# Kernel optimization log

Measured on AMD Instinct MI355X. Metric: run time of the kernel, lower is better.

## Reference

```python
import jax, jax.numpy as jnp
import numpy as np

# ---- straight-through binary quantizers (custom VJP matches torch autograd.Functions) ----
@jax.custom_vjp
def bq(x):
    return jnp.sign(x)
def _bq_fwd(x):
    return jnp.sign(x), x
def _bq_bwd(x, g):
    return (g * ((x > -1.0) & (x < 1.0)).astype(g.dtype),)
bq.defvjp(_bq_fwd, _bq_bwd)

@jax.custom_vjp
def bq_quad(x):
    return jnp.sign(x)
def _bqq_fwd(x):
    return jnp.sign(x), x
def _bqq_bwd(x, g):
    return (jnp.maximum(2.0 - jnp.abs(2.0 * x), 0.0) * g,)
bq_quad.defvjp(_bqq_fwd, _bqq_bwd)

def bilinear(x, W, s, b):
    # BiLinear: row-centered sign weights scaled by learned per-row factor, sign activations
    Wc = W - jnp.mean(W, axis=-1, keepdims=True)
    Wb = s * bq(Wc)                      # (out, in)
    return bq(x) @ Wb.T + b

def selective_scan(u, delta, A, Bs, Cs, D, delta_bias):
    # u, delta: (B,K,Dn,L); A: (K,Dn,N); Bs,Cs: (B,K,N,L); D, delta_bias: (K,Dn)
    Bn, K, Dn, L = u.shape
    N = A.shape[-1]
    delta = jax.nn.softplus(delta + delta_bias[None, :, :, None])
    def step(h, inp):
        ut, dt, Bt, Ct = inp             # (B,K,Dn),(B,K,Dn),(B,K,N),(B,K,N)
        dA = jnp.exp(dt[..., None] * A[None])
        h = dA * h + (dt * ut)[..., None] * Bt[:, :, None, :]
        y = jnp.einsum('bkdn,bkn->bkd', h, Ct)
        return h, y
    h0 = jnp.zeros((Bn, K, Dn, N), u.dtype)
    _, ys = jax.lax.scan(step, h0,
                         (u.transpose(3, 0, 1, 2), delta.transpose(3, 0, 1, 2),
                          Bs.transpose(3, 0, 1, 2), Cs.transpose(3, 0, 1, 2)))
    y = ys.transpose(1, 2, 3, 0)         # (B,K,Dn,L)
    return y + D[None, :, :, None] * u

def _forward(x, W_in, b_in, s_in, move0_b, conv_W, conv_b, rp_b0, prelu_a, rp_b1,
             Wl, bl, sl, Wd, bd, sd, dt_bias, A_logs, Ds, ln_w, ln_b, W_out, b_out, s_out):
    Bn, H, Wi, dm = x.shape
    Dn = conv_W.shape[0]
    K = 4
    N = A_logs.shape[1]
    R = Wd.shape[2]
    L = H * Wi
    xz = bilinear(x, W_in, s_in, b_in)                  # (B,H,W,2*Dn)
    xp, z = jnp.split(xz, 2, axis=-1)
    xc = xp.transpose(0, 3, 1, 2)                       # (B,Dn,H,W)
    # BConv2d: move0 bias -> sign (quad STE) -> binary conv -> RPReLU -> residual
    t = bq_quad(xc + move0_b[None, :, None, None])
    sc = jax.lax.stop_gradient(jnp.mean(jnp.abs(conv_W), axis=(1, 2, 3), keepdims=True))
    cw = jnp.clip(conv_W, -1.0, 1.0)
    Wb = jax.lax.stop_gradient(sc * jnp.sign(conv_W) - cw) + cw
    t = jax.lax.conv_general_dilated(t, Wb, (1, 1), [(1, 1), (1, 1)],
                                     dimension_numbers=('NCHW', 'OIHW', 'NCHW'))
    t = t + conv_b[None, :, None, None]
    t = t + rp_b0[None, :, None, None]
    t = jnp.where(t >= 0, t, prelu_a[None, :, None, None] * t)
    t = t + rp_b1[None, :, None, None] + xc
    xconv = jax.nn.silu(t)
    # 4-direction scan inputs
    x_flat = xconv.reshape(Bn, Dn, L)
    x_tr = xconv.transpose(0, 1, 3, 2).reshape(Bn, Dn, L)
    x_hwwh = jnp.stack([x_flat, x_tr], axis=1)
    xs = jnp.concatenate([x_hwwh, jnp.flip(x_hwwh, axis=-1)], axis=1)   # (B,K,Dn,L)
    # NOTE: torch does .view(B,L,-1) on contiguous (B,Dn,L) slices = raw reshape (not transpose)
    xin = xs.reshape(Bn, K, L, Dn)
    x_dbl = jax.vmap(bilinear, in_axes=(1, 0, 0, 0), out_axes=1)(xin, Wl, sl, bl)  # (B,K,L,R+2N)
    x_dbl = x_dbl.transpose(0, 1, 3, 2)                                 # (B,K,R+2N,L)
    dts_r, Bs, Cs = jnp.split(x_dbl, [R, R + N], axis=2)
    dts_in = dts_r.reshape(Bn, K, L, R)  # raw reshape, matches torch .view
    dts = jax.vmap(bilinear, in_axes=(1, 0, 0, 0), out_axes=1)(dts_in, Wd, sd, bd)  # (B,K,L,Dn)
    dts = dts.transpose(0, 1, 3, 2)                                     # (B,K,Dn,L)
    A = -jnp.exp(A_logs).reshape(K, Dn, N)
    out_y = selective_scan(xs, dts, A, Bs, Cs, Ds.reshape(K, Dn), dt_bias.reshape(K, Dn))
    inv_y = jnp.flip(out_y[:, 2:4], axis=-1)
    wh_y = out_y[:, 1].reshape(Bn, Dn, Wi, H).transpose(0, 1, 3, 2).reshape(Bn, Dn, L)
    invwh_y = inv_y[:, 1].reshape(Bn, Dn, Wi, H).transpose(0, 1, 3, 2).reshape(Bn, Dn, L)
    y = out_y[:, 0] + inv_y[:, 0] + wh_y + invwh_y                      # (B,Dn,L)
    y = y.transpose(0, 2, 1).reshape(Bn, H, Wi, Dn)
    mu = jnp.mean(y, axis=-1, keepdims=True)
    var = jnp.var(y, axis=-1, keepdims=True)
    y = (y - mu) / jnp.sqrt(var + 1e-5) * ln_w + ln_b                   # LayerNorm eps=1e-5
    y = y * jax.nn.silu(z)
    return bilinear(y, W_out, s_out, b_out)

def setup_inputs():
    key = jax.random.key(0)
    ks = jax.random.split(key, 12)
    B, H, Wi, dm = 4, 64, 64, 96
    Dn, N, R, K = 192, 16, 6, 4
    u = lambda k, sh, a: jax.random.uniform(k, sh, jnp.float32, -a, a)
    x = jax.random.normal(ks[0], (B, H, Wi, dm), jnp.float32)
    W_in = u(ks[1], (2 * Dn, dm), 0.015)
    b_in = u(ks[2], (2 * Dn,), 0.01)
    s_in = jnp.mean(jnp.abs(W_in), axis=1, keepdims=True)
    move0_b = jnp.zeros((Dn,), jnp.float32)
    conv_W = 0.05 * jax.random.normal(ks[3], (Dn, Dn, 3, 3), jnp.float32)
    conv_b = u(ks[4], (Dn,), 0.01)
    rp_b0 = jnp.zeros((Dn,), jnp.float32)
    prelu_a = 0.25 * jnp.ones((Dn,), jnp.float32)
    rp_b1 = jnp.zeros((Dn,), jnp.float32)
    Wl = u(ks[5], (K, R + 2 * N, Dn), 0.015)
    bl = u(ks[6], (K, R + 2 * N), 0.01)
    sl = jnp.mean(jnp.abs(Wl), axis=2, keepdims=True)
    std = R ** -0.5
    Wd = u(ks[7], (K, Dn, R), std)
    bd = u(ks[8], (K, Dn), 0.01)
    sd = jnp.mean(jnp.abs(Wd), axis=2, keepdims=True)
    dt = jnp.exp(jax.random.uniform(ks[9], (K * Dn,), jnp.float32)
                 * (np.log(0.1) - np.log(0.001)) + np.log(0.001))
    dt = jnp.clip(dt, 1e-4, None)
    dt_bias = dt + jnp.log(-jnp.expm1(-dt))
    A_logs = jnp.tile(jnp.log(jnp.arange(1, N + 1, dtype=jnp.float32))[None, :], (K * Dn, 1))
    Ds = jnp.ones((K * Dn,), jnp.float32)
    ln_w = jnp.ones((Dn,), jnp.float32)
    ln_b = jnp.zeros((Dn,), jnp.float32)
    W_out = u(ks[10], (dm, Dn), 0.015)
    b_out = u(ks[11], (dm,), 0.01)
    s_out = jnp.mean(jnp.abs(W_out), axis=1, keepdims=True)
    return dict(x=x, W_in=W_in, b_in=b_in, s_in=s_in, move0_b=move0_b, conv_W=conv_W,
                conv_b=conv_b, rp_b0=rp_b0, prelu_a=prelu_a, rp_b1=rp_b1, Wl=Wl, bl=bl,
                sl=sl, Wd=Wd, bd=bd, sd=sd, dt_bias=dt_bias, A_logs=A_logs, Ds=Ds,
                ln_w=ln_w, ln_b=ln_b, W_out=W_out, b_out=b_out, s_out=s_out)

def reference(x, W_in, b_in, s_in, move0_b, conv_W, conv_b, rp_b0, prelu_a, rp_b1,
              Wl, bl, sl, Wd, bd, sd, dt_bias, A_logs, Ds, ln_w, ln_b, W_out, b_out, s_out):
    return _forward(x, W_in, b_in, s_in, move0_b, conv_W, conv_b, rp_b0, prelu_a, rp_b1,
                    Wl, bl, sl, Wd, bd, sd, dt_bias, A_logs, Ds, ln_w, ln_b, W_out, b_out, s_out)
```

## Files before the change

kernel.cpp:

```cpp
#include <hip/hip_runtime.h>
#include <math.h>
#include <stdint.h>

#define BB 4
#define HH 64
#define WW2 64
#define DM 96
#define DN 192
#define KK 4
#define NN 16
#define RR 6
#define LL 4096
#define RN 38

#define LOG2E 1.4426950408889634f
#define LN2   0.6931471805599453f

#define OFF_WDB      0
#define OFF_WCS      4608
#define OFF_WAUX     15360
#define OFF_WSC      16896
#define OFF_WBIB     17088
#define OFF_WOUTB    18240
#define OFF_WLBB     18816
#define OFF_XBP      19728
#define OFF_PXS      19728
#define OFF_PXIN     412944
#define OFF_XP       462096
#define OFF_XCONV    3607824
#define OFF_XCT      6753552
#define OFF_HEND     462096
#define OFF_YA       9899280
#define OFF_SSUM     22482192

#define PLANE 4356
#define NCH 128
#define CHUNK 32

__device__ __forceinline__ float softplusf(float v) {
  return fmaxf(v, 0.f) + LN2 * log2f(1.f + exp2f(-fabsf(v) * LOG2E));
}
__device__ __forceinline__ float siluf(float v) {
  return v / (1.f + expf(-v));
}
__device__ __forceinline__ float waveAllSum(float s) {
  #pragma unroll
  for (int off = 32; off; off >>= 1) s += __shfl_xor(s, off, 64);
  return s;
}

__global__ __launch_bounds__(64) void k_prep(
    const float* __restrict__ W_in, const float* __restrict__ s_in,
    const float* __restrict__ W_out, const float* __restrict__ s_out,
    const float* __restrict__ Wl, const float* __restrict__ sl,
    const float* __restrict__ Wd, const float* __restrict__ sd,
    const float* __restrict__ convW, float* __restrict__ ws) {
  __shared__ float srow[1728];
  int r = blockIdx.x, lane = threadIdx.x;
  if (r < 384) {
    const float* row = W_in + r * DM;
    float s = 0.f;
    for (int c = lane; c < DM; c += 64) s += row[c];
    s = waveAllSum(s);
    float mean = s / (float)DM;
    if (lane < 3) {
      uint32_t wv = 0;
      #pragma unroll
      for (int i = 0; i < 32; ++i) wv |= (row[lane * 32 + i] - mean > 0.f ? 1u : 0u) << i;
      ((uint32_t*)(ws + OFF_WBIB))[r * 3 + lane] = wv;
    }
  } else if (r < 480) {
    int m = r - 384;
    const float* row = W_out + m * DN;
    float s = 0.f;
    for (int c = lane; c < DN; c += 64) s += row[c];
    s = waveAllSum(s);
    float mean = s / (float)DN;
    if (lane < 6) {
      uint32_t wv = 0;
      #pragma unroll
      for (int i = 0; i < 32; ++i) wv |= (row[lane * 32 + i] - mean > 0.f ? 1u : 0u) << i;
      ((uint32_t*)(ws + OFF_WOUTB))[m * 6 + lane] = wv;
    }
  } else if (r < 632) {
    int idx = r - 480;
    const float* row = Wl + idx * DN;
    float s = 0.f;
    for (int c = lane; c < DN; c += 64) s += row[c];
    s = waveAllSum(s);
    float mean = s / (float)DN;
    if (lane < 6) {
      uint32_t wv = 0;
      #pragma unroll
      for (int i = 0; i < 32; ++i) wv |= (row[lane * 32 + i] - mean > 0.f ? 1u : 0u) << i;
      ((uint32_t*)(ws + OFF_WLBB))[idx * 6 + lane] = wv;
    }
  } else if (r < 1400) {
    int idx = r - 632;
    const float* row = Wd + idx * RR;
    float s = (lane < RR) ? row[lane] : 0.f;
    s = waveAllSum(s);
    float mean = s / (float)RR;
    unsigned long long mb = __ballot((lane < RR) && (row[lane] - mean > 0.f));
    if (lane == 0) {
      ((uint32_t*)(ws + OFF_WDB))[idx] = (uint32_t)mb & 0x3Fu;
      (ws + OFF_WDB)[768 + idx] = sd[idx];
    }
  } else if (r < 1592) {
    int o = r - 1400;
    const float* row = convW + o * 1728;
    float s = 0.f;
    for (int j = lane; j < 1728; j += 64) {
      float v = row[j];
      srow[j] = v;
      s += fabsf(v);
    }
    s = waveAllSum(s);
    __syncthreads();
    float sc = s / 1728.f;
    uint32_t* wb = (uint32_t*)(ws + OFF_WCS);
    int* aux = (int*)(ws + OFF_WAUX);
    float* scf = ws + OFF_WSC;
    uint32_t word = 0;
    if (lane < 54) {
      int cw = lane / 9, tap = lane % 9;
      #pragma unroll
      for (int i = 0; i < 32; ++i)
        word |= (srow[(cw * 32 + i) * 9 + tap] > 0.f ? 1u : 0u) << i;
      wb[o * 56 + lane] = word;
    } else if (lane < 56) {
      wb[o * 56 + lane] = 0u;
    }
    int pc = (lane < 54) ? 2 * (int)__popc(word) - 32 : 0;
    int tapid = lane % 9;
    int wst = 0;
    #pragma unroll
    for (int cw = 0; cw < 6; ++cw) wst += __shfl(pc, cw * 9 + tapid, 64);
    int w_t[9];
    #pragma unroll
    for (int t9 = 0; t9 < 9; ++t9) w_t[t9] = __shfl(wst, t9, 64);
    if (lane == 0) {
      aux[o * 8 + 0] = w_t[0] + w_t[3] + w_t[6];
      aux[o * 8 + 1] = w_t[2] + w_t[5] + w_t[8];
      aux[o * 8 + 2] = w_t[0] + w_t[1] + w_t[2];
      aux[o * 8 + 3] = w_t[6] + w_t[7] + w_t[8];
      aux[o * 8 + 4] = w_t[0];
      aux[o * 8 + 5] = w_t[2];
      aux[o * 8 + 6] = w_t[6];
      aux[o * 8 + 7] = w_t[8];
      scf[o] = sc;
    }
  } else {
    int p = r - 1592;
    uint32_t* plane = (uint32_t*)(ws + OFF_XBP) + (size_t)p * PLANE;
    for (int i = lane; i < 66; i += 64) {
      plane[i] = 0u;
      plane[65 * 66 + i] = 0u;
    }
    for (int i = lane; i < 64; i += 64) {
      plane[(i + 1) * 66] = 0u;
      plane[(i + 1) * 66 + 65] = 0u;
    }
  }
}

__global__ __launch_bounds__(384) void k_bilin_in(
    const float* __restrict__ x, const float* __restrict__ b_in,
    const float* __restrict__ s_in, const float* __restrict__ move0,
    const float* __restrict__ ws, float* __restrict__ xp,
    uint32_t* __restrict__ pxin, uint32_t* __restrict__ xb) {
  __shared__ uint32_t spx[16 * 3];
  __shared__ float sxz[192 * 17];
  __shared__ float smv[DN];
  int p0 = blockIdx.x * 16;
  if (threadIdx.x < 48) {
    int pix = threadIdx.x / 3, wd = threadIdx.x % 3;
    const float* base = x + (size_t)(p0 + pix) * DM + wd * 32;
    uint32_t wv = 0;
    #pragma unroll
    for (int i = 0; i < 32; ++i) wv |= (base[i] > 0.f ? 1u : 0u) << i;
    spx[pix * 3 + wd] = wv;
  }
  if (threadIdx.x < DN) smv[threadIdx.x] = move0[threadIdx.x];
  __syncthreads();
  int half = threadIdx.x / 192;
  int o = threadIdx.x - half * 192;
  uint32_t w0, w1, w2;
  {
    const uint32_t* wb = (const uint32_t*)(ws + OFF_WBIB) + o * 3;
    w0 = wb[0]; w1 = wb[1]; w2 = wb[2];
  }
  float bias = b_in[o], sc = s_in[o];
  #pragma unroll
  for (int pp = 0; pp < 8; ++pp) {
    int pix = half * 8 + pp;
    int P = (int)__popc(spx[pix * 3 + 0] ^ w0) + (int)__popc(spx[pix * 3 + 1] ^ w1) +
            (int)__popc(spx[pix * 3 + 2] ^ w2);
    sxz[o * 17 + pix] = bias + sc * (float)(DM - 2 * P);
  }
  __syncthreads();
  int b = p0 >> 12, l0 = p0 & 4095;
  for (int f = threadIdx.x; f < DN * 16; f += 384) {
    int od = f >> 4, pix = f & 15;
    xp[((size_t)(b * DN + od)) * LL + l0 + pix] = sxz[od * 17 + pix];
  }
  if (threadIdx.x < 48) {
    int pix = threadIdx.x / 3, wd = threadIdx.x % 3;
    pxin[(size_t)(p0 + pix) * 3 + wd] = spx[pix * 3 + wd];
  }
  if (threadIdx.x < 96) {
    int pix = threadIdx.x / 6, cw = threadIdx.x % 6;
    uint32_t wv = 0;
    #pragma unroll
    for (int i = 0; i < 32; ++i) {
      int dch = cw * 32 + i;
      wv |= ((sxz[dch * 17 + pix] + smv[dch] > 0.f) ? 1u : 0u) << i;
    }
    int l = l0 + pix, h = l >> 6, w = l & 63;
    uint32_t* plane = xb + (size_t)(b * 6 + cw) * PLANE;
    plane[(h + 1) * 66 + 1 + w] = wv;
  }
}

__global__ __launch_bounds__(256) void k_conv(
    const uint32_t* __restrict__ xb, const float* __restrict__ xc,
    const uint32_t* __restrict__ wbits, const int* __restrict__ aux,
    const float* __restrict__ scf, const float* __restrict__ conv_b,
    const float* __restrict__ rp_b0, const float* __restrict__ prelu_a,
    const float* __restrict__ rp_b1, float* __restrict__ xconv) {
  int og = blockIdx.x & 3;
  int stripe = (blockIdx.x >> 2) & 15;
  int b = blockIdx.x >> 6;
  int w = threadIdx.x & 63, r = threadIdx.x >> 6;
  int h = stripe * 4 + r;

  __shared__ uint32_t swb[48 * 56];
  __shared__ int saux[48 * 8];
  __shared__ float sconst[48 * 4];
  for (int i = threadIdx.x; i < 48 * 56; i += 256) swb[i] = wbits[og * (48 * 56) + i];
  for (int i = threadIdx.x; i < 48 * 8; i += 256) saux[i] = aux[og * (48 * 8) + i];
  if (threadIdx.x < 48) {
    int o = og * 48 + threadIdx.x;
    sconst[threadIdx.x * 4 + 0] = scf[o];
    sconst[threadIdx.x * 4 + 1] = conv_b[o] + rp_b0[o];
    sconst[threadIdx.x * 4 + 2] = prelu_a[o];
    sconst[threadIdx.x * 4 + 3] = rp_b1[o];
  }

  uint32_t xw[6][9];
  const uint32_t* xpb = xb + (size_t)b * 6 * PLANE;
  #pragma unroll
  for (int cw = 0; cw < 6; ++cw) {
    const uint32_t* plane = xpb + cw * PLANE + (h + 1) * 66 + (w + 1);
    #pragma unroll
    for (int dy = 0; dy < 3; ++dy) {
      #pragma unroll
      for (int dx = 0; dx < 3; ++dx)
        xw[cw][dy * 3 + dx] = plane[(dy - 1) * 66 + (dx - 1)];
    }
  }
  bool isL = (w == 0), isR = (w == 63);
  bool isT = (h == 0), isB = (h == 63);
  const float* xcp = xc + ((size_t)(b * DN + og * 48)) * LL + h * 64 + w;
  float* xop = xconv + ((size_t)(b * DN + og * 48)) * LL + h * 64 + w;
  __syncthreads();

  #pragma unroll 1
  for (int oc = 0; oc < 48; ++oc) {
    const uint32_t* wp = &swb[oc * 56];
    int P = 0;
    #pragma unroll
    for (int cw = 0; cw < 6; ++cw) {
      int pp = 0;
      #pragma unroll
      for (int t = 0; t < 9; ++t) pp += (int)__popc(wp[cw * 9 + t] ^ xw[cw][t]);
      P += pp;
    }
    int corr = isL ? saux[oc * 8 + 0] : (isR ? saux[oc * 8 + 1] : 0);
    if (isT) {
      corr += saux[oc * 8 + 2];
      if (isL) corr -= saux[oc * 8 + 4];
      if (isR) corr -= saux[oc * 8 + 5];
    }
    if (isB) {
      corr += saux[oc * 8 + 3];
      if (isL) corr -= saux[oc * 8 + 6];
      if (isR) corr -= saux[oc * 8 + 7];
    }
    float acc = sconst[oc * 4 + 0] * (float)(1728 - 2 * P + corr);
    float t = acc + sconst[oc * 4 + 1];
    t = (t >= 0.f) ? t : sconst[oc * 4 + 2] * t;
    t += sconst[oc * 4 + 3] + *xcp;
    *xop = siluf(t);
    xcp += LL; xop += LL;
  }
}

__global__ __launch_bounds__(256) void k_build_bits(const float* __restrict__ xconv,
                                                    uint32_t* __restrict__ pxs) {
  __shared__ float tile[64][65];
  int bd = blockIdx.x;
  int b = bd / DN, dch = bd - b * DN;
  const float* img = xconv + (size_t)bd * LL;
  for (int i = threadIdx.x; i < LL; i += 256)
    tile[i >> 6][i & 63] = img[i];
  __syncthreads();
  int lane = threadIdx.x & 63;
  #pragma unroll
  for (int k = 0; k < 4; ++k) {
    size_t wbase = ((size_t)((b * KK + k) * DN + dch)) * 128;
    for (int j = threadIdx.x; j < LL; j += 256) {
      float v;
      if (k == 0)      v = tile[j >> 6][j & 63];
      else if (k == 1) v = tile[j & 63][j >> 6];
      else if (k == 2) { int t2 = 4095 - j; v = tile[t2 >> 6][t2 & 63]; }
      else             { int t2 = 4095 - j; v = tile[t2 & 63][t2 >> 6]; }
      unsigned long long m = __ballot(v > 0.f);
      if (lane == 0)       pxs[wbase + (j >> 5)] = (uint32_t)m;
      else if (lane == 32) pxs[wbase + (j >> 5)] = (uint32_t)(m >> 32);
    }
  }
}

__global__ __launch_bounds__(256) void k_xpose(const float* __restrict__ xconv,
                                               float* __restrict__ xct) {
  __shared__ float tile[64][65];
  int ts = blockIdx.x & 63;
  int rest = blockIdx.x >> 6;
  int dg = rest % 3;
  int b = rest / 3;
  int d0 = dg * 64, t0 = ts * 64;
  for (int i = threadIdx.x; i < 4096; i += 256) {
    int dd = i >> 6, tt = i & 63;
    tile[dd][tt] = xconv[((size_t)(b * DN + d0 + dd)) * LL + t0 + tt];
  }
  __syncthreads();
  for (int i = threadIdx.x; i < 4096; i += 256) {
    int tt = i >> 6, dd = i & 63;
    xct[((size_t)(b * LL + t0 + tt)) * DN + d0 + dd] = tile[dd][tt];
  }
}

__device__ __forceinline__ void rpowers(float r, float* a) {
  float r2 = r * r, r3 = r2 * r, r4 = r2 * r2, r8 = r4 * r4;
  a[0] = r;       a[1] = r2;      a[2] = r3;      a[3] = r4;
  a[4] = r4 * r;  a[5] = r4 * r2; a[6] = r4 * r3; a[7] = r8;
  a[8] = r8 * r;  a[9] = r8 * r2; a[10] = r8 * r3; a[11] = r8 * r4;
  a[12] = r8 * a[4]; a[13] = r8 * a[5]; a[14] = r8 * a[6]; a[15] = r8 * r8;
}

__global__ __launch_bounds__(192) void k_scan_a(
    const float* __restrict__ xct, const uint32_t* __restrict__ pxs,
    const float* __restrict__ ws, const float* __restrict__ bl,
    const float* __restrict__ sl, const float* __restrict__ bd,
    const float* __restrict__ dt_bias, const float* __restrict__ A_logs,
    const float* __restrict__ Ds, float* __restrict__ yA,
    float* __restrict__ hend, float* __restrict__ Ssum) {
  int c = blockIdx.x & (NCH - 1);
  int bk = blockIdx.x >> 7;
  int k = bk & 3, b = bk >> 2;
  int d = threadIdx.x;
  int t0 = c << 5;
  __shared__ uint32_t sdtm[CHUNK];
  __shared__ uint32_t spxr[CHUNK * 6];
  __shared__ uint32_t swl[RN * 6];
  __shared__ float sblv[RN], sslv[RN];
  __shared__ float4 sB4[CHUNK * 4];
  __shared__ float4 sC4[CHUNK * 4];
  __shared__ float sDV[7 * 192], sR[7 * 192];
  float* sBf = (float*)sB4;
  float* sCf = (float*)sC4;
  const uint32_t* ppx = pxs + (size_t)bk * 24576;
  spxr[d] = ppx[t0 * 6 + d];
  for (int i = d; i < RN * 6; i += 192) swl[i] = ((const uint32_t*)(ws + OFF_WLBB))[k * RN * 6 + i];
  if (d < RN) {
    sblv[d] = bl[k * RN + d];
    sslv[d] = sl[k * RN + d];
  }
  __syncthreads();
  if (d < CHUNK) {
    uint32_t m = 0;
    int fbase = (t0 + d) * 6;
    #pragma unroll
    for (int r = 0; r < 6; ++r) {
      int f = fbase + r;
      int o = f >> 12, l = f & 4095;
      const uint32_t* prow = ppx + l * 6;
      int P = 0;
      #pragma unroll
      for (int j = 0; j < 6; ++j) P += (int)__popc(prow[j] ^ swl[o * 6 + j]);
      float val = sblv[o] + sslv[o] * (float)(DN - 2 * P);
      m |= (val > 0.f ? 1u : 0u) << r;
    }
    sdtm[d] = m;
  }
  for (int i = d; i < CHUNK * 32; i += 192) {
    int t = i >> 5, nn = i & 31;
    int o = RR + nn;
    int P = 0;
    #pragma unroll
    for (int j = 0; j < 6; ++j) P += (int)__popc(spxr[t * 6 + j] ^ swl[o * 6 + j]);
    float val = sblv[o] + sslv[o] * (float)(DN - 2 * P);
    if (nn < 16) sBf[t * 16 + nn] = val;
    else         sCf[t * 16 + (nn - 16)] = val;
  }
  uint32_t w6 = ((const uint32_t*)(ws + OFF_WDB))[k * DN + d];
  float sdv = (ws + OFF_WDB)[768 + k * DN + d];
  float biasd = bd[k * DN + d] + dt_bias[k * DN + d];
  float Dd = Ds[k * DN + d];
  #pragma unroll
  for (int pc = 0; pc < 7; ++pc) {
    float dv = softplusf(biasd + sdv * (float)(RR - 2 * pc));
    sDV[pc * 192 + d] = dv;
    sR[pc * 192 + d] = exp2f(-dv * LOG2E);
  }
  float Araw[16];
  bool fok = true;
  {
    const float* ap = A_logs + (k * DN + d) * NN;
    #pragma unroll
    for (int n = 0; n < NN; ++n) {
      Araw[n] = -expf(ap[n]);
      fok = fok && (fabsf(Araw[n] + (float)(n + 1)) < 1e-3f);
    }
  }
  bool fastpath = (__ballot(fok) == ~0ull);
  float An[16];
  if (!fastpath) {
    #pragma unroll
    for (int n = 0; n < NN; ++n) An[n] = Araw[n] * LOG2E;
  }
  float h[16];
  #pragma unroll
  for (int n = 0; n < NN; ++n) h[n] = 0.f;
  float S = 0.f;
  int ubase = b * (LL * DN) + d;
  int ybase = bk * (LL * DN) + d;
  __syncthreads();
  #pragma unroll 1
  for (int seg = 0; seg < 4; ++seg) {
    float uu[8];
    int r192[8];
    #pragma unroll
    for (int i = 0; i < 8; ++i) {
      int t = t0 + seg * 8 + i;
      int r = (k >= 2) ? (4095 - t) : t;
      if (k & 1) r = ((r & 63) << 6) | (r >> 6);
      r192[i] = r * DN;
      uu[i] = xct[ubase + r192[i]];
    }
    #pragma unroll
    for (int i = 0; i < 8; ++i) {
      int t = seg * 8 + i;
      float uv = uu[i];
      int pc = (int)__popc(sdtm[t] ^ w6);
      float dv = sDV[pc * 192 + d];
      S += dv;
      float du = dv * uv;
      float yv = Dd * uv;
      if (fastpath) {
        float rv = sR[pc * 192 + d];
        float a[16];
        rpowers(rv, a);
        #pragma unroll
        for (int g = 0; g < 4; ++g) {
          float4 bv = sB4[t * 4 + g];
          float4 cv = sC4[t * 4 + g];
          h[4 * g + 0] = a[4 * g + 0] * h[4 * g + 0] + du * bv.x;
          h[4 * g + 1] = a[4 * g + 1] * h[4 * g + 1] + du * bv.y;
          h[4 * g + 2] = a[4 * g + 2] * h[4 * g + 2] + du * bv.z;
          h[4 * g + 3] = a[4 * g + 3] * h[4 * g + 3] + du * bv.w;
          yv += cv.x * h[4 * g + 0];
          yv += cv.y * h[4 * g + 1];
          yv += cv.z * h[4 * g + 2];
          yv += cv.w * h[4 * g + 3];
        }
      } else {
        #pragma unroll
        for (int g = 0; g < 4; ++g) {
          float4 bv = sB4[t * 4 + g];
          float4 cv = sC4[t * 4 + g];
          float a0 = exp2f(dv * An[4 * g + 0]);
          float a1 = exp2f(dv * An[4 * g + 1]);
          float a2 = exp2f(dv * An[4 * g + 2]);
          float a3 = exp2f(dv * An[4 * g + 3]);
          h[4 * g + 0] = a0 * h[4 * g + 0] + du * bv.x;
          h[4 * g + 1] = a1 * h[4 * g + 1] + du * bv.y;
          h[4 * g + 2] = a2 * h[4 * g + 2] + du * bv.z;
          h[4 * g + 3] = a3 * h[4 * g + 3] + du * bv.w;
          yv += cv.x * h[4 * g + 0];
          yv += cv.y * h[4 * g + 1];
          yv += cv.z * h[4 * g + 2];
          yv += cv.w * h[4 * g + 3];
        }
      }
      yA[ybase + r192[i]] = yv;
    }
  }
  float* hp = hend + (size_t)c * 49152 + (size_t)(bk * DN + d) * 16;
  #pragma unroll
  for (int n = 0; n < NN; n += 4)
    *(float4*)(hp + n) = make_float4(h[n], h[n + 1], h[n + 2], h[n + 3]);
  Ssum[c * 3072 + bk * DN + d] = S;
}

__global__ __launch_bounds__(256) void k_scan_b(
    const float* __restrict__ A_logs, const float* __restrict__ Ssum,
    float* __restrict__ hend) {
  int tid = blockIdx.x * 256 + threadIdx.x;
  int bkd = tid >> 4, n = tid & 15;
  int bk = bkd / DN, d = bkd - bk * DN;
  int k = bk & 3;
  float An2 = -expf(A_logs[(k * DN + d) * NN + n]) * LOG2E;
  float h = 0.f;
  float Sc = Ssum[bkd];
  float he = hend[tid];
  #pragma unroll 1
  for (int c = 0; c < NCH; ++c) {
    float Sn = 0.f, hn = 0.f;
    if (c < NCH - 1) {
      Sn = Ssum[(c + 1) * 3072 + bkd];
      hn = hend[(size_t)(c + 1) * 49152 + tid];
    }
    hend[(size_t)c * 49152 + tid] = h;
    h = exp2f(An2 * Sc) * h + he;
    Sc = Sn; he = hn;
  }
}

__global__ __launch_bounds__(192) void k_scan_corr(
    float* __restrict__ yA, const uint32_t* __restrict__ pxs,
    const float* __restrict__ ws, const float* __restrict__ bl,
    const float* __restrict__ sl, const float* __restrict__ bd,
    const float* __restrict__ dt_bias, const float* __restrict__ A_logs,
    const float* __restrict__ h0buf) {
  int c = blockIdx.x & (NCH - 1);
  if (c == 0) return;
  int bk = blockIdx.x >> 7;
  int k = bk & 3;
  int d = threadIdx.x;
  int t0 = c << 5;
  __shared__ uint32_t sdtm[CHUNK];
  __shared__ uint32_t spxr[CHUNK * 6];
  __shared__ uint32_t swl[RN * 6];
  __shared__ float sblv[RN], sslv[RN];
  __shared__ float4 sC4[CHUNK * 4];
  __shared__ float sDV[7 * 192];
  float* sCf = (float*)sC4;
  const uint32_t* ppx = pxs + (size_t)bk * 24576;
  spxr[d] = ppx[t0 * 6 + d];
  for (int i = d; i < RN * 6; i += 192) swl[i] = ((const uint32_t*)(ws + OFF_WLBB))[k * RN * 6 + i];
  if (d < RN) {
    sblv[d] = bl[k * RN + d];
    sslv[d] = sl[k * RN + d];
  }
  __syncthreads();
  if (d < CHUNK) {
    uint32_t m = 0;
    int fbase = (t0 + d) * 6;
    #pragma unroll
    for (int r = 0; r < 6; ++r) {
      int f = fbase + r;
      int o = f >> 12, l = f & 4095;
      const uint32_t* prow = ppx + l * 6;
      int P = 0;
      #pragma unroll
      for (int j = 0; j < 6; ++j) P += (int)__popc(prow[j] ^ swl[o * 6 + j]);
      float val = sblv[o] + sslv[o] * (float)(DN - 2 * P);
      m |= (val > 0.f ? 1u : 0u) << r;
    }
    sdtm[d] = m;
  }
  for (int i = d; i < CHUNK * 16; i += 192) {
    int t = i >> 4, n = i & 15;
    int o = RR + NN + n;
    int P = 0;
    #pragma unroll
    for (int j = 0; j < 6; ++j) P += (int)__popc(spxr[t * 6 + j] ^ swl[o * 6 + j]);
    sCf[t * 16 + n] = sblv[o] + sslv[o] * (float)(DN - 2 * P);
  }
  uint32_t w6 = ((const uint32_t*)(ws + OFF_WDB))[k * DN + d];
  float sdv = (ws + OFF_WDB)[768 + k * DN + d];
  float biasd = bd[k * DN + d] + dt_bias[k * DN + d];
  #pragma unroll
  for (int pc = 0; pc < 7; ++pc)
    sDV[pc * 192 + d] = softplusf(biasd + sdv * (float)(RR - 2 * pc));
  float Araw[16];
  bool fok = true;
  {
    const float* ap = A_logs + (k * DN + d) * NN;
    #pragma unroll
    for (int n = 0; n < NN; ++n) {
      Araw[n] = -expf(ap[n]);
      fok = fok && (fabsf(Araw[n] + (float)(n + 1)) < 1e-3f);
    }
  }
  bool fastpath = (__ballot(fok) == ~0ull);
  float An[16];
  if (!fastpath) {
    #pragma unroll
    for (int n = 0; n < NN; ++n) An[n] = Araw[n] * LOG2E;
  }
  float h0[16];
  {
    const float* hp = h0buf + (size_t)c * 49152 + (size_t)(bk * DN + d) * 16;
    #pragma unroll
    for (int n = 0; n < NN; n += 4) {
      float4 v = *(const float4*)(hp + n);
      h0[n] = v.x; h0[n + 1] = v.y; h0[n + 2] = v.z; h0[n + 3] = v.w;
    }
  }
  float S = 0.f;
  int ybase = bk * (LL * DN) + d;
  __syncthreads();
  #pragma unroll 1
  for (int seg = 0; seg < 4; ++seg) {
    float yy[8];
    int r192[8];
    #pragma unroll
    for (int i = 0; i < 8; ++i) {
      int t = t0 + seg * 8 + i;
      int r = (k >= 2) ? (4095 - t) : t;
      if (k & 1) r = ((r & 63) << 6) | (r >> 6);
      r192[i] = r * DN;
      yy[i] = yA[ybase + r192[i]];
    }
    #pragma unroll
    for (int i = 0; i < 8; ++i) {
      int t = seg * 8 + i;
      int pc = (int)__popc(sdtm[t] ^ w6);
      S += sDV[pc * 192 + d];
      float yv = 0.f;
      if (fastpath) {
        float rho = exp2f(-S * LOG2E);
        float a[16];
        rpowers(rho, a);
        #pragma unroll
        for (int g = 0; g < 4; ++g) {
          float4 cv = sC4[t * 4 + g];
          yv += cv.x * (a[4 * g + 0] * h0[4 * g + 0]);
          yv += cv.y * (a[4 * g + 1] * h0[4 * g + 1]);
          yv += cv.z * (a[4 * g + 2] * h0[4 * g + 2]);
          yv += cv.w * (a[4 * g + 3] * h0[4 * g + 3]);
        }
      } else {
        #pragma unroll
        for (int g = 0; g < 4; ++g) {
          float4 cv = sC4[t * 4 + g];
          yv += cv.x * (exp2f(S * An[4 * g + 0]) * h0[4 * g + 0]);
          yv += cv.y * (exp2f(S * An[4 * g + 1]) * h0[4 * g + 1]);
          yv += cv.z * (exp2f(S * An[4 * g + 2]) * h0[4 * g + 2]);
          yv += cv.w * (exp2f(S * An[4 * g + 3]) * h0[4 * g + 3]);
        }
      }
      yA[ybase + r192[i]] = yy[i] + yv;
    }
  }
}

__global__ __launch_bounds__(256) void k_ln_out(
    const float* __restrict__ yA, const uint32_t* __restrict__ pxin,
    const float* __restrict__ b_in, const float* __restrict__ s_in,
    const float* __restrict__ ln_w, const float* __restrict__ ln_b,
    const float* __restrict__ ws, const float* __restrict__ b_out,
    const float* __restrict__ s_out, float* __restrict__ out) {
  __shared__ float ty[64 * 193];
  __shared__ float ps[256];
  __shared__ float smu[64], srs[64];
  __shared__ float slw[DN], slb[DN];
  __shared__ uint32_t ybits[64 * 6];
  __shared__ uint32_t swo[96 * 6];
  __shared__ float sb[96], ssc[96];
  __shared__ uint32_t szw[DN * 3];
  __shared__ float szb[DN], szs[DN];
  __shared__ uint32_t spxt[64 * 3];
  int b = blockIdx.x >> 6;
  int l0 = (blockIdx.x & 63) << 6;
  if (threadIdx.x < DN) {
    slw[threadIdx.x] = ln_w[threadIdx.x];
    slb[threadIdx.x] = ln_b[threadIdx.x];
    szb[threadIdx.x] = b_in[DN + threadIdx.x];
    szs[threadIdx.x] = s_in[DN + threadIdx.x];
  }
  for (int i = threadIdx.x; i < 96 * 6; i += 256) swo[i] = ((const uint32_t*)(ws + OFF_WOUTB))[i];
  for (int i = threadIdx.x; i < DN * 3; i += 256) szw[i] = ((const uint32_t*)(ws + OFF_WBIB))[DN * 3 + i];
  if (threadIdx.x < 96) {
    sb[threadIdx.x] = b_out[threadIdx.x];
    ssc[threadIdx.x] = s_out[threadIdx.x];
  }
  for (int i = threadIdx.x; i < 192; i += 256) spxt[i] = pxin[(size_t)(b * LL + l0) * 3 + i];
  const float* y0 = yA + (size_t)(b * 4 + 0) * (LL * DN) + (size_t)l0 * DN;
  const float* y1 = yA + (size_t)(b * 4 + 1) * (LL * DN) + (size_t)l0 * DN;
  const float* y2 = yA + (size_t)(b * 4 + 2) * (LL * DN) + (size_t)l0 * DN;
  const float* y3 = yA + (size_t)(b * 4 + 3) * (LL * DN) + (size_t)l0 * DN;
  for (int i = threadIdx.x; i < 64 * DN; i += 256) {
    int lc = i / DN, dd = i - lc * DN;
    size_t off = (size_t)lc * DN + dd;
    ty[lc * 193 + dd] = y0[off] + y1[off] + y2[off] + y3[off];
  }
  __syncthreads();
  int lc = threadIdx.x & 63, part = threadIdx.x >> 6;
  float s = 0.f;
  for (int d = part * 48; d < part * 48 + 48; ++d) s += ty[lc * 193 + d];
  ps[threadIdx.x] = s;
  __syncthreads();
  if (threadIdx.x < 64)
    smu[threadIdx.x] = (ps[threadIdx.x] + ps[threadIdx.x + 64] +
                        ps[threadIdx.x + 128] + ps[threadIdx.x + 192]) / (float)DN;
  __syncthreads();
  float mu = smu[lc];
  float q = 0.f;
  for (int d = part * 48; d < part * 48 + 48; ++d) {
    float v = ty[lc * 193 + d] - mu; q += v * v;
  }
  ps[threadIdx.x] = q;
  __syncthreads();
  if (threadIdx.x < 64) {
    float var = (ps[threadIdx.x] + ps[threadIdx.x + 64] +
                 ps[threadIdx.x + 128] + ps[threadIdx.x + 192]) / (float)DN;
    srs[threadIdx.x] = rsqrtf(var + 1e-5f);
  }
  __syncthreads();
  for (int item = threadIdx.x; item < 64 * 6; item += 256) {
    int lc2 = item / 6, wd = item - (item / 6) * 6;
    float mu2 = smu[lc2], rs2 = srs[lc2];
    uint32_t px0 = spxt[lc2 * 3 + 0], px1 = spxt[lc2 * 3 + 1], px2 = spxt[lc2 * 3 + 2];
    uint32_t wv = 0;
    #pragma unroll
    for (int i = 0; i < 32; ++i) {
      int dd = wd * 32 + i;
      float lnv = (ty[lc2 * 193 + dd] - mu2) * rs2 * slw[dd] + slb[dd];
      int P = (int)__popc(px0 ^ szw[dd * 3 + 0]) + (int)__popc(px1 ^ szw[dd * 3 + 1]) +
              (int)__popc(px2 ^ szw[dd * 3 + 2]);
      float zv = szb[dd] + szs[dd] * (float)(DM - 2 * P);
      wv |= ((lnv * zv > 0.f) ? 1u : 0u) << i;
    }
    ybits[lc2 * 6 + wd] = wv;
  }
  __syncthreads();
  float* op = out + (size_t)(b * LL + l0) * DM;
  for (int oi = threadIdx.x; oi < 64 * DM; oi += 256) {
    int pr = oi / DM, m = oi % DM;
    int P = 0;
    #pragma unroll
    for (int j = 0; j < 6; ++j) P += (int)__popc(ybits[pr * 6 + j] ^ swo[m * 6 + j]);
    op[(size_t)pr * DM + m] = sb[m] + ssc[m] * (float)(DN - 2 * P);
  }
}

extern "C" void kernel_launch(void* const* d_in, const int* in_sizes, int n_in,
                              void* d_out, int out_size, void* d_ws, size_t ws_size,
                              hipStream_t stream) {
  const float* x       = (const float*)d_in[0];
  const float* W_in    = (const float*)d_in[1];
  const float* b_in    = (const float*)d_in[2];
  const float* s_in    = (const float*)d_in[3];
  const float* move0_b = (const float*)d_in[4];
  const float* conv_W  = (const float*)d_in[5];
  const float* conv_b  = (const float*)d_in[6];
  const float* rp_b0   = (const float*)d_in[7];
  const float* prelu_a = (const float*)d_in[8];
  const float* rp_b1   = (const float*)d_in[9];
  const float* Wl      = (const float*)d_in[10];
  const float* bl      = (const float*)d_in[11];
  const float* sl      = (const float*)d_in[12];
  const float* Wd      = (const float*)d_in[13];
  const float* bd      = (const float*)d_in[14];
  const float* sd      = (const float*)d_in[15];
  const float* dt_bias = (const float*)d_in[16];
  const float* A_logs  = (const float*)d_in[17];
  const float* Ds      = (const float*)d_in[18];
  const float* ln_w    = (const float*)d_in[19];
  const float* ln_b    = (const float*)d_in[20];
  const float* W_out   = (const float*)d_in[21];
  const float* b_out   = (const float*)d_in[22];
  const float* s_out   = (const float*)d_in[23];
  float* ws  = (float*)d_ws;
  float* out = (float*)d_out;

  hipLaunchKernelGGL(k_prep, dim3(1616), dim3(64), 0, stream,
                     W_in, s_in, W_out, s_out, Wl, sl, Wd, sd, conv_W, ws);
  hipLaunchKernelGGL(k_bilin_in, dim3(1024), dim3(384), 0, stream,
                     x, b_in, s_in, move0_b, ws, ws + OFF_XP,
                     (uint32_t*)(ws + OFF_PXIN), (uint32_t*)(ws + OFF_XBP));
  hipLaunchKernelGGL(k_conv, dim3(256), dim3(256), 0, stream,
                     (const uint32_t*)(ws + OFF_XBP), ws + OFF_XP,
                     (const uint32_t*)(ws + OFF_WCS), (const int*)(ws + OFF_WAUX),
                     ws + OFF_WSC, conv_b, rp_b0, prelu_a, rp_b1,
                     ws + OFF_XCONV);
  hipLaunchKernelGGL(k_build_bits, dim3(768), dim3(256), 0, stream,
                     ws + OFF_XCONV, (uint32_t*)(ws + OFF_PXS));
  hipLaunchKernelGGL(k_xpose, dim3(768), dim3(256), 0, stream,
                     ws + OFF_XCONV, ws + OFF_XCT);
  hipLaunchKernelGGL(k_scan_a, dim3(2048), dim3(192), 0, stream,
                     ws + OFF_XCT, (const uint32_t*)(ws + OFF_PXS), ws, bl, sl,
                     bd, dt_bias, A_logs, Ds, ws + OFF_YA, ws + OFF_HEND,
                     ws + OFF_SSUM);
  hipLaunchKernelGGL(k_scan_b, dim3(192), dim3(256), 0, stream,
                     A_logs, ws + OFF_SSUM, ws + OFF_HEND);
  hipLaunchKernelGGL(k_scan_corr, dim3(2048), dim3(192), 0, stream,
                     ws + OFF_YA, (const uint32_t*)(ws + OFF_PXS), ws, bl, sl,
                     bd, dt_bias, A_logs, ws + OFF_HEND);
  hipLaunchKernelGGL(k_ln_out, dim3(256), dim3(256), 0, stream,
                     ws + OFF_YA, (const uint32_t*)(ws + OFF_PXIN), b_in, s_in,
                     ln_w, ln_b, ws, b_out, s_out, out);
}
```

Before: 324.7 us.

## Split conv and LN-out grids finer and merge bit-build with transpose kernel

The binary conv kernel now splits each 48-channel group into four 12-channel sub-blocks, growing the grid from 256 to 1024 blocks. The LayerNorm/output kernel processes 16 positions per block instead of 64, also giving 1024 blocks, with the reductions reworked to 16-way partial sums. The bit-packing and transpose kernels are merged into one launch that dispatches on block index. The aim is to fill the GPU's compute units better on small grids and to save one launch. The cost is that conv blocks now reload the 54-word input bit window per thread four times as often.

```diff
diff --git a/kernel.cpp b/kernel.cpp
--- a/kernel.cpp
+++ b/kernel.cpp
@@ -228,19 +228,21 @@
     const float* __restrict__ scf, const float* __restrict__ conv_b,
     const float* __restrict__ rp_b0, const float* __restrict__ prelu_a,
     const float* __restrict__ rp_b1, float* __restrict__ xconv) {
-  int og = blockIdx.x & 3;
-  int stripe = (blockIdx.x >> 2) & 15;
-  int b = blockIdx.x >> 6;
+  int ocg = blockIdx.x & 3;
+  int og = (blockIdx.x >> 2) & 3;
+  int stripe = (blockIdx.x >> 4) & 15;
+  int b = blockIdx.x >> 8;
   int w = threadIdx.x & 63, r = threadIdx.x >> 6;
   int h = stripe * 4 + r;
-
-  __shared__ uint32_t swb[48 * 56];
-  __shared__ int saux[48 * 8];
-  __shared__ float sconst[48 * 4];
-  for (int i = threadIdx.x; i < 48 * 56; i += 256) swb[i] = wbits[og * (48 * 56) + i];
-  for (int i = threadIdx.x; i < 48 * 8; i += 256) saux[i] = aux[og * (48 * 8) + i];
-  if (threadIdx.x < 48) {
-    int o = og * 48 + threadIdx.x;
+  int obase = og * 48 + ocg * 12;
+
+  __shared__ uint32_t swb[12 * 56];
+  __shared__ int saux[12 * 8];
+  __shared__ float sconst[12 * 4];
+  for (int i = threadIdx.x; i < 12 * 56; i += 256) swb[i] = wbits[obase * 56 + i];
+  for (int i = threadIdx.x; i < 12 * 8; i += 256) saux[i] = aux[obase * 8 + i];
+  if (threadIdx.x < 12) {
+    int o = obase + threadIdx.x;
     sconst[threadIdx.x * 4 + 0] = scf[o];
     sconst[threadIdx.x * 4 + 1] = conv_b[o] + rp_b0[o];
     sconst[threadIdx.x * 4 + 2] = prelu_a[o];
@@ -261,12 +263,12 @@
   }
   bool isL = (w == 0), isR = (w == 63);
   bool isT = (h == 0), isB = (h == 63);
-  const float* xcp = xc + ((size_t)(b * DN + og * 48)) * LL + h * 64 + w;
-  float* xop = xconv + ((size_t)(b * DN + og * 48)) * LL + h * 64 + w;
+  const float* xcp = xc + ((size_t)(b * DN + obase)) * LL + h * 64 + w;
+  float* xop = xconv + ((size_t)(b * DN + obase)) * LL + h * 64 + w;
   __syncthreads();
 
   #pragma unroll 1
-  for (int oc = 0; oc < 48; ++oc) {
+  for (int oc = 0; oc < 12; ++oc) {
     const uint32_t* wp = &swb[oc * 56];
     int P = 0;
     #pragma unroll
@@ -296,48 +298,48 @@
   }
 }
 
-__global__ __launch_bounds__(256) void k_build_bits(const float* __restrict__ xconv,
-                                                    uint32_t* __restrict__ pxs) {
+__global__ __launch_bounds__(256) void k_bits_xpose(const float* __restrict__ xconv,
+                                                    uint32_t* __restrict__ pxs,
+                                                    float* __restrict__ xct) {
   __shared__ float tile[64][65];
-  int bd = blockIdx.x;
-  int b = bd / DN, dch = bd - b * DN;
-  const float* img = xconv + (size_t)bd * LL;
-  for (int i = threadIdx.x; i < LL; i += 256)
-    tile[i >> 6][i & 63] = img[i];
-  __syncthreads();
-  int lane = threadIdx.x & 63;
-  #pragma unroll
-  for (int k = 0; k < 4; ++k) {
-    size_t wbase = ((size_t)((b * KK + k) * DN + dch)) * 128;
-    for (int j = threadIdx.x; j < LL; j += 256) {
-      float v;
-      if (k == 0)      v = tile[j >> 6][j & 63];
-      else if (k == 1) v = tile[j & 63][j >> 6];
-      else if (k == 2) { int t2 = 4095 - j; v = tile[t2 >> 6][t2 & 63]; }
-      else             { int t2 = 4095 - j; v = tile[t2 & 63][t2 >> 6]; }
-      unsigned long long m = __ballot(v > 0.f);
-      if (lane == 0)       pxs[wbase + (j >> 5)] = (uint32_t)m;
-      else if (lane == 32) pxs[wbase + (j >> 5)] = (uint32_t)(m >> 32);
-    }
-  }
-}
-
-__global__ __launch_bounds__(256) void k_xpose(const float* __restrict__ xconv,
-                                               float* __restrict__ xct) {
-  __shared__ float tile[64][65];
-  int ts = blockIdx.x & 63;
-  int rest = blockIdx.x >> 6;
-  int dg = rest % 3;
-  int b = rest / 3;
-  int d0 = dg * 64, t0 = ts * 64;
-  for (int i = threadIdx.x; i < 4096; i += 256) {
-    int dd = i >> 6, tt = i & 63;
-    tile[dd][tt] = xconv[((size_t)(b * DN + d0 + dd)) * LL + t0 + tt];
-  }
-  __syncthreads();
-  for (int i = threadIdx.x; i < 4096; i += 256) {
-    int tt = i >> 6, dd = i & 63;
-    xct[((size_t)(b * LL + t0 + tt)) * DN + d0 + dd] = tile[dd][tt];
+  if (blockIdx.x < 768) {
+    int bd = blockIdx.x;
+    int b = bd / DN, dch = bd - b * DN;
+    const float* img = xconv + (size_t)bd * LL;
+    for (int i = threadIdx.x; i < LL; i += 256)
+      tile[i >> 6][i & 63] = img[i];
+    __syncthreads();
+    int lane = threadIdx.x & 63;
+    #pragma unroll
+    for (int k = 0; k < 4; ++k) {
+      size_t wbase = ((size_t)((b * KK + k) * DN + dch)) * 128;
+      for (int j = threadIdx.x; j < LL; j += 256) {
+        float v;
+        if (k == 0)      v = tile[j >> 6][j & 63];
+        else if (k == 1) v = tile[j & 63][j >> 6];
+        else if (k == 2) { int t2 = 4095 - j; v = tile[t2 >> 6][t2 & 63]; }
+        else             { int t2 = 4095 - j; v = tile[t2 & 63][t2 >> 6]; }
+        unsigned long long m = __ballot(v > 0.f);
+        if (lane == 0)       pxs[wbase + (j >> 5)] = (uint32_t)m;
+        else if (lane == 32) pxs[wbase + (j >> 5)] = (uint32_t)(m >> 32);
+      }
+    }
+  } else {
+    int idx = blockIdx.x - 768;
+    int ts = idx & 63;
+    int rest = idx >> 6;
+    int dg = rest % 3;
+    int b = rest / 3;
+    int d0 = dg * 64, t0 = ts * 64;
+    for (int i = threadIdx.x; i < 4096; i += 256) {
+      int dd = i >> 6, tt = i & 63;
+      tile[dd][tt] = xconv[((size_t)(b * DN + d0 + dd)) * LL + t0 + tt];
+    }
+    __syncthreads();
+    for (int i = threadIdx.x; i < 4096; i += 256) {
+      int tt = i >> 6, dd = i & 63;
+      xct[((size_t)(b * LL + t0 + tt)) * DN + d0 + dd] = tile[dd][tt];
+    }
   }
 }
 
@@ -664,18 +666,18 @@
     const float* __restrict__ ln_w, const float* __restrict__ ln_b,
     const float* __restrict__ ws, const float* __restrict__ b_out,
     const float* __restrict__ s_out, float* __restrict__ out) {
-  __shared__ float ty[64 * 193];
+  __shared__ float ty[16 * 193];
   __shared__ float ps[256];
-  __shared__ float smu[64], srs[64];
+  __shared__ float smu[16], srs[16];
   __shared__ float slw[DN], slb[DN];
-  __shared__ uint32_t ybits[64 * 6];
+  __shared__ uint32_t ybits[16 * 6];
   __shared__ uint32_t swo[96 * 6];
   __shared__ float sb[96], ssc[96];
   __shared__ uint32_t szw[DN * 3];
   __shared__ float szb[DN], szs[DN];
-  __shared__ uint32_t spxt[64 * 3];
-  int b = blockIdx.x >> 6;
-  int l0 = (blockIdx.x & 63) << 6;
+  __shared__ uint32_t spxt[16 * 3];
+  int b = blockIdx.x >> 8;
+  int l0 = (blockIdx.x & 255) << 4;
   if (threadIdx.x < DN) {
     slw[threadIdx.x] = ln_w[threadIdx.x];
     slb[threadIdx.x] = ln_b[threadIdx.x];
@@ -688,41 +690,45 @@
     sb[threadIdx.x] = b_out[threadIdx.x];
     ssc[threadIdx.x] = s_out[threadIdx.x];
   }
-  for (int i = threadIdx.x; i < 192; i += 256) spxt[i] = pxin[(size_t)(b * LL + l0) * 3 + i];
+  if (threadIdx.x < 48) spxt[threadIdx.x] = pxin[(size_t)(b * LL + l0) * 3 + threadIdx.x];
   const float* y0 = yA + (size_t)(b * 4 + 0) * (LL * DN) + (size_t)l0 * DN;
   const float* y1 = yA + (size_t)(b * 4 + 1) * (LL * DN) + (size_t)l0 * DN;
   const float* y2 = yA + (size_t)(b * 4 + 2) * (LL * DN) + (size_t)l0 * DN;
   const float* y3 = yA + (size_t)(b * 4 + 3) * (LL * DN) + (size_t)l0 * DN;
-  for (int i = threadIdx.x; i < 64 * DN; i += 256) {
+  for (int i = threadIdx.x; i < 16 * DN; i += 256) {
     int lc = i / DN, dd = i - lc * DN;
     size_t off = (size_t)lc * DN + dd;
     ty[lc * 193 + dd] = y0[off] + y1[off] + y2[off] + y3[off];
   }
   __syncthreads();
-  int lc = threadIdx.x & 63, part = threadIdx.x >> 6;
+  int lc = threadIdx.x & 15, part = threadIdx.x >> 4;
   float s = 0.f;
-  for (int d = part * 48; d < part * 48 + 48; ++d) s += ty[lc * 193 + d];
+  for (int d = part * 12; d < part * 12 + 12; ++d) s += ty[lc * 193 + d];
   ps[threadIdx.x] = s;
   __syncthreads();
-  if (threadIdx.x < 64)
-    smu[threadIdx.x] = (ps[threadIdx.x] + ps[threadIdx.x + 64] +
-                        ps[threadIdx.x + 128] + ps[threadIdx.x + 192]) / (float)DN;
+  if (threadIdx.x < 16) {
+    float m = 0.f;
+    #pragma unroll
+    for (int p = 0; p < 16; ++p) m += ps[p * 16 + threadIdx.x];
+    smu[threadIdx.x] = m / (float)DN;
+  }
   __syncthreads();
   float mu = smu[lc];
   float q = 0.f;
-  for (int d = part * 48; d < part * 48 + 48; ++d) {
+  for (int d = part * 12; d < part * 12 + 12; ++d) {
     float v = ty[lc * 193 + d] - mu; q += v * v;
   }
   ps[threadIdx.x] = q;
   __syncthreads();
-  if (threadIdx.x < 64) {
-    float var = (ps[threadIdx.x] + ps[threadIdx.x + 64] +
-                 ps[threadIdx.x + 128] + ps[threadIdx.x + 192]) / (float)DN;
-    srs[threadIdx.x] = rsqrtf(var + 1e-5f);
-  }
-  __syncthreads();
-  for (int item = threadIdx.x; item < 64 * 6; item += 256) {
-    int lc2 = item / 6, wd = item - (item / 6) * 6;
+  if (threadIdx.x < 16) {
+    float vv = 0.f;
+    #pragma unroll
+    for (int p = 0; p < 16; ++p) vv += ps[p * 16 + threadIdx.x];
+    srs[threadIdx.x] = rsqrtf(vv / (float)DN + 1e-5f);
+  }
+  __syncthreads();
+  if (threadIdx.x < 16 * 6) {
+    int lc2 = threadIdx.x / 6, wd = threadIdx.x % 6;
     float mu2 = smu[lc2], rs2 = srs[lc2];
     uint32_t px0 = spxt[lc2 * 3 + 0], px1 = spxt[lc2 * 3 + 1], px2 = spxt[lc2 * 3 + 2];
     uint32_t wv = 0;
@@ -739,7 +745,7 @@
   }
   __syncthreads();
   float* op = out + (size_t)(b * LL + l0) * DM;
-  for (int oi = threadIdx.x; oi < 64 * DM; oi += 256) {
+  for (int oi = threadIdx.x; oi < 16 * DM; oi += 256) {
     int pr = oi / DM, m = oi % DM;
     int P = 0;
     #pragma unroll
@@ -783,15 +789,13 @@
   hipLaunchKernelGGL(k_bilin_in, dim3(1024), dim3(384), 0, stream,
                      x, b_in, s_in, move0_b, ws, ws + OFF_XP,
                      (uint32_t*)(ws + OFF_PXIN), (uint32_t*)(ws + OFF_XBP));
-  hipLaunchKernelGGL(k_conv, dim3(256), dim3(256), 0, stream,
+  hipLaunchKernelGGL(k_conv, dim3(1024), dim3(256), 0, stream,
                      (const uint32_t*)(ws + OFF_XBP), ws + OFF_XP,
                      (const uint32_t*)(ws + OFF_WCS), (const int*)(ws + OFF_WAUX),
                      ws + OFF_WSC, conv_b, rp_b0, prelu_a, rp_b1,
                      ws + OFF_XCONV);
-  hipLaunchKernelGGL(k_build_bits, dim3(768), dim3(256), 0, stream,
-                     ws + OFF_XCONV, (uint32_t*)(ws + OFF_PXS));
-  hipLaunchKernelGGL(k_xpose, dim3(768), dim3(256), 0, stream,
-                     ws + OFF_XCONV, ws + OFF_XCT);
+  hipLaunchKernelGGL(k_bits_xpose, dim3(1536), dim3(256), 0, stream,
+                     ws + OFF_XCONV, (uint32_t*)(ws + OFF_PXS), ws + OFF_XCT);
   hipLaunchKernelGGL(k_scan_a, dim3(2048), dim3(192), 0, stream,
                      ws + OFF_XCT, (const uint32_t*)(ws + OFF_PXS), ws, bl, sl,
                      bd, dt_bias, A_logs, Ds, ws + OFF_YA, ws + OFF_HEND,
@@ -801,7 +805,7 @@
   hipLaunchKernelGGL(k_scan_corr, dim3(2048), dim3(192), 0, stream,
                      ws + OFF_YA, (const uint32_t*)(ws + OFF_PXS), ws, bl, sl,
                      bd, dt_bias, A_logs, ws + OFF_HEND);
-  hipLaunchKernelGGL(k_ln_out, dim3(256), dim3(256), 0, stream,
+  hipLaunchKernelGGL(k_ln_out, dim3(1024), dim3(256), 0, stream,
                      ws + OFF_YA, (const uint32_t*)(ws + OFF_PXIN), b_in, s_in,
                      ln_w, ln_b, ws, b_out, s_out, out);
 }
```

Result: faster. 304.3 us (-6.3%).
